# Kernel tuning notes

Hardware: AMD Instinct MI355X
Metric: run time of the kernel (lower is better)

## Reference

```python
import jax, jax.numpy as jnp
import numpy as np

LARGE_CONSTANT = 1e9


def setup_inputs() -> dict:
    key = jax.random.key(0)
    ks = jax.random.split(key, 8)
    B, S, D, U = 8, 2048, 1024, 1024
    scale = 1.0 / np.sqrt(D)
    inputs_1 = jax.random.normal(ks[0], (B, S, D), dtype=jnp.float32)
    inputs_2 = jax.random.normal(ks[1], (B, S, D), dtype=jnp.float32)
    Wq = jax.random.normal(ks[2], (D, U), dtype=jnp.float32) * scale
    Wk = jax.random.normal(ks[3], (D, U), dtype=jnp.float32) * scale
    Wv = jax.random.normal(ks[4], (D, U), dtype=jnp.float32) * scale
    bq = jnp.zeros((U,), dtype=jnp.float32)
    bk = jnp.zeros((U,), dtype=jnp.float32)
    bv = jnp.zeros((U,), dtype=jnp.float32)
    # metric initialized as identity in the original; add small noise to exercise it
    metric = jnp.eye(U, dtype=jnp.float32) + 0.01 * jax.random.normal(ks[5], (U, U), dtype=jnp.float32)
    return {"inputs_1": inputs_1, "inputs_2": inputs_2, "Wq": Wq, "bq": bq,
            "Wk": Wk, "bk": bk, "Wv": Wv, "bv": bv, "metric": metric}


def reference(inputs_1, inputs_2, Wq, bq, Wk, bk, Wv, bv, metric):
    U = Wq.shape[1]
    scaling = jnp.sqrt(jnp.asarray(U, dtype=inputs_1.dtype))
    queries = inputs_1 @ Wq + bq            # [b, i, u]
    keys = inputs_2 @ Wk + bk               # [b, j, u]
    values = inputs_2 @ Wv + bv             # [b, j, u]
    queries = jnp.einsum('biu,uv->biv', queries, metric)  # learned-metric transform
    scores = jnp.einsum('biu,bju->bij', queries, keys) / scaling
    # causal mask: band_part(ones, -1, 0) is lower-triangular
    S = scores.shape[-1]
    causal = jnp.tril(jnp.ones((S, S), dtype=scores.dtype))
    scores = scores - LARGE_CONSTANT * (1.0 - causal)
    alpha = jax.nn.softmax(scores, axis=-1)
    return jnp.einsum('bij,bju->biu', alpha, values)
```

## Files before the change

kernel.cpp:

```cpp
#include <hip/hip_runtime.h>


#define Bq 8
#define Sq 2048
#define Dq 1024
#define Uq 1024

typedef __bf16 bf16;
typedef __bf16 bf16x8 __attribute__((ext_vector_type(8)));
typedef float f32x4 __attribute__((ext_vector_type(4)));
typedef unsigned short u16;
typedef unsigned int u32;

__device__ __forceinline__ u16 f2bf(float f) {
  u32 u = __builtin_bit_cast(u32, f);
  u32 r = u + 0x7fffu + ((u >> 16) & 1u);
  return (u16)(r >> 16);
}
__device__ __forceinline__ float bf2f(u32 h) {
  return __builtin_bit_cast(float, h << 16);
}

__device__ __forceinline__ void gl_lds16(const void* g, void* l) {
  __builtin_amdgcn_global_load_lds(
      (const __attribute__((address_space(1))) u32*)g,
      (__attribute__((address_space(3))) u32*)l, 16, 0, 0);
}


__global__ __launch_bounds__(256) void cvt_x(const float* __restrict__ x1,
                                             const float* __restrict__ x2,
                                             u16* __restrict__ o1,
                                             u16* __restrict__ o2, int n4) {
  int idx = blockIdx.x * 256 + threadIdx.x;
  if (idx >= n4) return;
  const float* in = blockIdx.y ? x2 : x1;
  u16* out = blockIdx.y ? o2 : o1;
  float4 v = ((const float4*)in)[idx];
  ushort4 o;
  o.x = f2bf(v.x); o.y = f2bf(v.y); o.z = f2bf(v.z); o.w = f2bf(v.w);
  ((ushort4*)out)[idx] = o;
}

__global__ __launch_bounds__(256) void cvt_bf16(const float* __restrict__ in,
                                                u16* __restrict__ out, int n4) {
  int idx = blockIdx.x * 256 + threadIdx.x;
  if (idx >= n4) return;
  float4 v = ((const float4*)in)[idx];
  ushort4 o;
  o.x = f2bf(v.x); o.y = f2bf(v.y); o.z = f2bf(v.z); o.w = f2bf(v.w);
  ((ushort4*)out)[idx] = o;
}

__global__ __launch_bounds__(256) void transpose_cvt3(
    const float* __restrict__ s0, u16* __restrict__ d0,
    const float* __restrict__ s1, u16* __restrict__ d1,
    const float* __restrict__ s2, u16* __restrict__ d2) {
  __shared__ float tile[32][33];
  const float* in = (blockIdx.z == 0) ? s0 : (blockIdx.z == 1) ? s1 : s2;
  u16* out = (blockIdx.z == 0) ? d0 : (blockIdx.z == 1) ? d1 : d2;
  const int N = 1024;
  int tx = threadIdx.x & 31, ty = threadIdx.x >> 5;
  int x0 = blockIdx.x * 32, y0 = blockIdx.y * 32;
#pragma unroll
  for (int r = 0; r < 32; r += 8)
    tile[ty + r][tx] = in[(size_t)(y0 + ty + r) * N + x0 + tx];
  __syncthreads();
#pragma unroll
  for (int r = 0; r < 32; r += 8)
    out[(size_t)(x0 + ty + r) * N + y0 + tx] = f2bf(tile[tx][ty + r]);
}

__global__ __launch_bounds__(256) void bqm_kernel(const float* __restrict__ bq,
                                                  const float* __restrict__ metric,
                                                  float* __restrict__ bqm) {
  int v = blockIdx.x * 256 + threadIdx.x;
  float s = 0.f;
  for (int u = 0; u < Uq; ++u) s += bq[u] * metric[(size_t)u * Uq + v];
  bqm[v] = s;
}

__global__ __launch_bounds__(256) void fill_zero(float4* __restrict__ p, int n4) {
  int i = blockIdx.x * 256 + threadIdx.x;
  if (i < n4) p[i] = float4{0.f, 0.f, 0.f, 0.f};
}

#define BM 128
#define BN 128
#define BK 32

template <int OUT_BF16, int BIAS>
__global__ __launch_bounds__(256) void gemm_tn(
    const bf16* __restrict__ A, const bf16* __restrict__ B, void* __restrict__ Cv,
    const float* __restrict__ bias, int lda, int ldb, int ldc,
    long long sA, long long sB, long long sC, int K,
    int causal_skip, int causal_klimit) {
  __shared__ __align__(16) bf16 lA[3][BM * BK];
  __shared__ __align__(16) bf16 lB[3][BN * BK];
  int bx = causal_klimit ? (gridDim.x - 1 - blockIdx.x) : blockIdx.x;
  int m0 = bx * BM, n0 = blockIdx.y * BN;
  if (causal_skip && n0 > m0 + BM - 1) return;
  long long b = blockIdx.z;
  A += b * sA;
  B += b * sB;
  int t = threadIdx.x;
  int w = t >> 6, l = t & 63;
  int wr = (w >> 1) * 64, wc = (w & 1) * 64;
  int Kend = causal_klimit ? min(K, m0 + BM) : K;
  int nk = Kend / BK;

  f32x4 acc[4][4] = {};
  int rowA = t >> 2, kc = (t & 3) * 8;
  int lm = l & 15, q = l >> 4;

  const bf16* gA = A + (long long)(m0 + rowA) * lda + kc;
  const bf16* gB = B + (long long)(n0 + rowA) * ldb + kc;
  long long a64 = (long long)64 * lda, b64 = (long long)64 * ldb;

  auto stage = [&](int kt, int buf) {
    int k0 = kt * BK;
    char* dA = (char*)lA[buf] + w * 1024;
    char* dB = (char*)lB[buf] + w * 1024;
    gl_lds16(gA + k0, dA);
    gl_lds16(gA + k0 + a64, dA + 4096);
    gl_lds16(gB + k0, dB);
    gl_lds16(gB + k0 + b64, dB + 4096);
  };

  stage(0, 0);
  stage(1, 1);
  int cur = 0;
  for (int kt = 0; kt < nk; ++kt) {
    if (kt + 2 < nk) {
      int pb = cur + 2;
      if (pb >= 3) pb -= 3;
      stage(kt + 2, pb);
      asm volatile("s_waitcnt vmcnt(8)\n\ts_barrier" ::: "memory");
    } else if (kt + 1 < nk) {
      asm volatile("s_waitcnt vmcnt(4)\n\ts_barrier" ::: "memory");
    } else {
      asm volatile("s_waitcnt vmcnt(0)\n\ts_barrier" ::: "memory");
    }
    bf16x8 af[4], bfr[4];
#pragma unroll
    for (int i = 0; i < 4; ++i)
      af[i] = *(const bf16x8*)&lA[cur][(wr + i * 16 + lm) * BK + q * 8];
#pragma unroll
    for (int i = 0; i < 4; ++i)
      bfr[i] = *(const bf16x8*)&lB[cur][(wc + i * 16 + lm) * BK + q * 8];
#pragma unroll
    for (int i = 0; i < 4; ++i)
#pragma unroll
      for (int j = 0; j < 4; ++j)
        acc[i][j] = __builtin_amdgcn_mfma_f32_16x16x32_bf16(af[i], bfr[j], acc[i][j], 0, 0, 0);
    asm volatile("s_barrier" ::: "memory");
    cur = (cur == 2) ? 0 : cur + 1;
  }

  char* Cb = (char*)Cv + (OUT_BF16 ? b * sC * 2 : b * sC * 4);
#pragma unroll
  for (int i = 0; i < 4; ++i) {
#pragma unroll
    for (int j = 0; j < 4; ++j) {
      int col = n0 + wc + j * 16 + lm;
      float bc = (BIAS == 1) ? bias[col] : 0.f;
#pragma unroll
      for (int r = 0; r < 4; ++r) {
        int row = m0 + wr + i * 16 + q * 4 + r;
        float v = acc[i][j][r] + bc;
        if (BIAS == 2) v += bias[row];
        size_t idx = (size_t)row * ldc + col;
        if (OUT_BF16)
          ((u16*)Cb)[idx] = f2bf(v);
        else
          ((float*)Cb)[idx] = v;
      }
    }
  }
}


#define GBODY(P, CLO, CB, NLO, NB)                                             \
  {                                                                            \
    const int rp_ = (P) & 3, rn_ = ((P) + 1) & 3;                              \
    if ((P) + 3 < NP) stage((P) + 3);                                          \
    const bf16* pa_ = pAl + rp_ * 8192;                                        \
    _Pragma("unroll") for (int i = 0; i < 4; ++i)                              \
        aHi[i] = *(const bf16x8*)(pa_ + (i + 4) * 512);                        \
    __builtin_amdgcn_s_setprio(1);                                             \
    _Pragma("unroll") for (int i = 0; i < 4; ++i)                              \
        _Pragma("unroll") for (int j = 0; j < 4; ++j)                          \
            acc[i][j] = __builtin_amdgcn_mfma_f32_16x16x32_bf16(               \
                CLO[i], CB[j], acc[i][j], 0, 0, 0);                            \
    __builtin_amdgcn_s_setprio(0);                                             \
    if ((P) + 1 < NP) {                                                        \
      const bf16* pa2_ = pAl + rn_ * 8192;                                     \
      const bf16* pb2_ = pBl + rn_ * 8192;                                     \
      _Pragma("unroll") for (int i = 0; i < 4; ++i)                            \
          NLO[i] = *(const bf16x8*)(pa2_ + i * 512);                           \
      _Pragma("unroll") for (int j = 0; j < 4; ++j)                            \
          NB[j] = *(const bf16x8*)(pb2_ + j * 512);                            \
    }                                                                          \
    __builtin_amdgcn_s_setprio(1);                                             \
    _Pragma("unroll") for (int i = 0; i < 4; ++i)                              \
        _Pragma("unroll") for (int j = 0; j < 4; ++j)                          \
            acc[i + 4][j] = __builtin_amdgcn_mfma_f32_16x16x32_bf16(           \
                aHi[i], CB[j], acc[i + 4][j], 0, 0, 0);                        \
    __builtin_amdgcn_s_setprio(0);                                             \
    if ((P) + 3 < NP)                                                          \
      asm volatile("s_waitcnt vmcnt(4) lgkmcnt(0)\n\ts_barrier" ::: "memory"); \
    else if ((P) + 2 < NP)                                                     \
      asm volatile("s_waitcnt vmcnt(0) lgkmcnt(0)\n\ts_barrier" ::: "memory"); \
  }

template <int OUT_BF16, int BIAS>
__global__ __launch_bounds__(512, 2) void gemm_tn256(
    const bf16* __restrict__ A, const bf16* __restrict__ B, void* __restrict__ Cv,
    const float* __restrict__ bias, int lda, int ldb, int ldc,
    long long sA, long long sB, long long sC, int K,
    int causal_skip, int causal_klimit) {
  __shared__ __align__(16) bf16 lA[4][256 * 32];
  __shared__ __align__(16) bf16 lB[4][256 * 32];
  int bx = causal_klimit ? (gridDim.x - 1 - blockIdx.x) : blockIdx.x;
  int m0 = bx * 256, n0 = blockIdx.y * 256;
  if (causal_skip && n0 > m0 + 255) return;
  long long b = blockIdx.z;
  A += b * sA;
  B += b * sB;
  int t = threadIdx.x;
  int w = t >> 6, l = t & 63;
  int wr = w >> 2, wc = w & 3;
  int lm = l & 15, q = l >> 4;
  int cq = q ^ ((lm >> 1) & 3);

  int Kend = causal_klimit ? min(K, m0 + 256) : K;
  int NP = Kend >> 5;

  int r0 = t >> 2;
  int c0 = t & 3;
  int q0 = c0 ^ ((r0 >> 1) & 3);
  const bf16* gA0 = A + (long long)(m0 + r0) * lda + q0 * 8;
  const bf16* gA1 = gA0 + (long long)128 * lda;
  const bf16* gB0 = B + (long long)(n0 + r0) * ldb + q0 * 8;
  const bf16* gB1 = gB0 + (long long)128 * ldb;
  char* dA = (char*)&lA[0][0] + w * 1024;
  char* dB = (char*)&lB[0][0] + w * 1024;

  auto stage = [&](int ph) {
    int reg_ = ph & 3;
    int k0 = ph << 5;
    char* da = dA + reg_ * 16384;
    char* db = dB + reg_ * 16384;
    gl_lds16(gA0 + k0, da);
    gl_lds16(gA1 + k0, da + 8192);
    gl_lds16(gB0 + k0, db);
    gl_lds16(gB1 + k0, db + 8192);
  };

  const bf16* pAl = &lA[0][0] + (wr * 128 + lm) * 32 + cq * 8;
  const bf16* pBl = &lB[0][0] + (wc * 64 + lm) * 32 + cq * 8;

  f32x4 acc[8][4] = {};
  bf16x8 aLoA[4], bFrA[4], aLoB[4], bFrB[4], aHi[4];

  stage(0); stage(1); stage(2);
  asm volatile("s_waitcnt vmcnt(8)\n\ts_barrier" ::: "memory");
#pragma unroll
  for (int i = 0; i < 4; ++i) aLoA[i] = *(const bf16x8*)(pAl + i * 512);
#pragma unroll
  for (int j = 0; j < 4; ++j) bFrA[j] = *(const bf16x8*)(pBl + j * 512);
  asm volatile("s_waitcnt vmcnt(4) lgkmcnt(0)\n\ts_barrier" ::: "memory");

  for (int p = 0; p < NP; p += 2) {
    GBODY(p, aLoA, bFrA, aLoB, bFrB)
    GBODY(p + 1, aLoB, bFrB, aLoA, bFrA)
  }

  char* Cb = (char*)Cv + (OUT_BF16 ? b * sC * 2 : b * sC * 4);
#pragma unroll
  for (int i = 0; i < 8; ++i) {
#pragma unroll
    for (int j = 0; j < 4; ++j) {
      int col = n0 + wc * 64 + j * 16 + lm;
      float bc = (BIAS == 1) ? bias[col] : 0.f;
#pragma unroll
      for (int r = 0; r < 4; ++r) {
        int row = m0 + wr * 128 + i * 16 + q * 4 + r;
        float v = acc[i][j][r] + bc;
        if (BIAS == 2) v += bias[row];
        size_t idxc = (size_t)row * ldc + col;
        if (OUT_BF16)
          ((u16*)Cb)[idxc] = f2bf(v);
        else
          ((float*)Cb)[idxc] = v;
      }
    }
  }
}

__global__ __launch_bounds__(256) void softmax_causal(u16* __restrict__ sc) {
  __shared__ __align__(16) float sm[Sq];
  __shared__ float red[8];
  int gr = blockIdx.x;
  int i = gr & (Sq - 1);
  u16* rowp = sc + (size_t)gr * Sq;
  int t = threadIdx.x;
  int nv = i + 1;
  int wlim = (i & ~255) + 256;
  int j0 = t * 8;
  if (j0 < nv) {
    uint4 pk = ((const uint4*)rowp)[t];
    float4 lo, hi;
    lo.x = bf2f(pk.x & 0xffffu); lo.y = bf2f(pk.x >> 16);
    lo.z = bf2f(pk.y & 0xffffu); lo.w = bf2f(pk.y >> 16);
    hi.x = bf2f(pk.z & 0xffffu); hi.y = bf2f(pk.z >> 16);
    hi.z = bf2f(pk.w & 0xffffu); hi.w = bf2f(pk.w >> 16);
    ((float4*)sm)[2 * t] = lo;
    ((float4*)sm)[2 * t + 1] = hi;
  }
  __syncthreads();
  const float scl = 0.03125f;
  float m = -1e30f;
  for (int j = t; j < nv; j += 256) m = fmaxf(m, sm[j]);
#pragma unroll
  for (int o = 32; o; o >>= 1) m = fmaxf(m, __shfl_xor(m, o));
  if ((t & 63) == 0) red[t >> 6] = m;
  __syncthreads();
  m = fmaxf(fmaxf(red[0], red[1]), fmaxf(red[2], red[3])) * scl;
  float sum = 0.f;
  for (int j = t; j < nv; j += 256) sum += __expf(sm[j] * scl - m);
#pragma unroll
  for (int o = 32; o; o >>= 1) sum += __shfl_xor(sum, o);
  if ((t & 63) == 0) red[4 + (t >> 6)] = sum;
  __syncthreads();
  float rinv = 1.0f / (red[4] + red[5] + red[6] + red[7]);
  if (j0 < wlim) {
    u16 ov[8];
#pragma unroll
    for (int k = 0; k < 8; ++k)
      ov[k] = (j0 + k < nv) ? f2bf(__expf(sm[j0 + k] * scl - m) * rinv) : (u16)0;
    uint4 po;
    po.x = (u32)ov[0] | ((u32)ov[1] << 16);
    po.y = (u32)ov[2] | ((u32)ov[3] << 16);
    po.z = (u32)ov[4] | ((u32)ov[5] << 16);
    po.w = (u32)ov[6] | ((u32)ov[7] << 16);
    ((uint4*)rowp)[t] = po;
  }
}


extern "C" void kernel_launch(void* const* d_in, const int* in_sizes, int n_in,
                              void* d_out, int out_size, void* d_ws, size_t ws_size,
                              hipStream_t stream) {
  const float* X1 = (const float*)d_in[0];
  const float* X2 = (const float*)d_in[1];
  const float* Wq = (const float*)d_in[2];
  const float* bq = (const float*)d_in[3];
  const float* Wk = (const float*)d_in[4];
  const float* bk = (const float*)d_in[5];
  const float* Wv = (const float*)d_in[6];
  const float* bv = (const float*)d_in[7];
  const float* metric = (const float*)d_in[8];
  float* out = (float*)d_out;

  const size_t XB = (size_t)Bq * Sq * Dq * 2;
  const size_t WB = (size_t)Dq * Uq * 2;
  const size_t NEED = 3 * XB + 5 * WB + 4096;

  if (ws_size < NEED) {
    fill_zero<<<(out_size / 4 + 255) / 256, 256, 0, stream>>>((float4*)d_out, out_size / 4);
    return;
  }

  char* ws = (char*)d_ws;
  bf16* X1b = (bf16*)(ws);
  bf16* X2b = (bf16*)(ws + XB);
  bf16* Vt = (bf16*)(ws + 2 * XB);
  bf16* WqB = (bf16*)(ws + 3 * XB);
  bf16* metT = (bf16*)(ws + 3 * XB + WB);
  bf16* WkT = (bf16*)(ws + 3 * XB + 2 * WB);
  bf16* WvT = (bf16*)(ws + 3 * XB + 3 * WB);
  bf16* WqmT = (bf16*)(ws + 3 * XB + 4 * WB);
  float* bqm = (float*)(ws + 3 * XB + 5 * WB);
  u16* Sc = (u16*)ws;
  bf16* Qb = (bf16*)d_out;
  bf16* Kb = (bf16*)d_out + (size_t)Bq * Sq * Uq;

  int nx4 = Bq * Sq * Dq / 4;
  cvt_x<<<dim3((nx4 + 255) / 256, 2), 256, 0, stream>>>(X1, X2, (u16*)X1b, (u16*)X2b, nx4);
  cvt_bf16<<<(Dq * Uq / 4 + 255) / 256, 256, 0, stream>>>(Wq, (u16*)WqB, Dq * Uq / 4);
  transpose_cvt3<<<dim3(32, 32, 3), 256, 0, stream>>>(
      metric, (u16*)metT, Wk, (u16*)WkT, Wv, (u16*)WvT);
  bqm_kernel<<<Uq / 256, 256, 0, stream>>>(bq, metric, bqm);

  gemm_tn<1, 0><<<dim3(Uq / BM, Dq / BN, 1), 256, 0, stream>>>(
      metT, WqB, WqmT, nullptr, Uq, Uq, Dq, 0, 0, 0, Uq, 0, 0);

  const int MQ = Bq * Sq;
  gemm_tn256<1, 1><<<dim3(MQ / 256, Uq / 256, 1), 512, 0, stream>>>(
      X1b, WqmT, Qb, bqm, Dq, Dq, Uq, 0, 0, 0, Dq, 0, 0);
  gemm_tn256<1, 1><<<dim3(MQ / 256, Uq / 256, 1), 512, 0, stream>>>(
      X2b, WkT, Kb, bk, Dq, Dq, Uq, 0, 0, 0, Dq, 0, 0);
  gemm_tn256<1, 2><<<dim3(Uq / 256, Sq / 256, Bq), 512, 0, stream>>>(
      WvT, X2b, Vt, bv, Dq, Dq, Sq, 0, (long long)Sq * Dq, (long long)Uq * Sq, Dq, 0, 0);

  gemm_tn256<1, 0><<<dim3(Sq / 256, Sq / 256, Bq), 512, 0, stream>>>(
      Qb, Kb, Sc, nullptr, Uq, Uq, Sq, (long long)Sq * Uq, (long long)Sq * Uq,
      (long long)Sq * Sq, Uq, 1, 0);

  softmax_causal<<<Bq * Sq, 256, 0, stream>>>(Sc);

  gemm_tn256<0, 0><<<dim3(Sq / 256, Uq / 256, Bq), 512, 0, stream>>>(
      (const bf16*)Sc, Vt, out, nullptr, Sq, Sq, Uq, (long long)Sq * Sq,
      (long long)Uq * Sq, (long long)Sq * Uq, Sq, 0, 1);

  (void)in_sizes; (void)n_in; (void)ws_size;
}
```

Baseline: 524.5 us.

## Split global-to-LDS staging across half-phases and split-K the weight-fold GEMM

The 256-tile GEMM main loop now issues half of each prefetch stage before and half after the first MFMA group, and places barriers between the two halves of every phase with finer vmcnt waits. The loop is unrolled four phases deep with compile-time LDS region indices. The intent is to spread memory traffic and shorten barrier stalls. Separately, the small metric×Wq GEMM is split along K into four atomic-add slices into an fp32 buffer, then converted to bf16, to expose more parallelism. This adds a zero-fill kernel and a conversion kernel, plus atomic traffic.

```diff
diff --git a/kernel.cpp b/kernel.cpp
--- a/kernel.cpp
+++ b/kernel.cpp
@@ -157,7 +157,7 @@
     cur = (cur == 2) ? 0 : cur + 1;
   }
 
-  char* Cb = (char*)Cv + (OUT_BF16 ? b * sC * 2 : b * sC * 4);
+  char* Cb = (char*)Cv + (OUT_BF16 == 1 ? b * sC * 2 : b * sC * 4);
 #pragma unroll
   for (int i = 0; i < 4; ++i) {
 #pragma unroll
@@ -170,8 +170,10 @@
         float v = acc[i][j][r] + bc;
         if (BIAS == 2) v += bias[row];
         size_t idx = (size_t)row * ldc + col;
-        if (OUT_BF16)
+        if (OUT_BF16 == 1)
           ((u16*)Cb)[idx] = f2bf(v);
+        else if (OUT_BF16 == 2)
+          unsafeAtomicAdd(&((float*)Cb)[idx], v);
         else
           ((float*)Cb)[idx] = v;
       }
@@ -180,37 +182,48 @@
 }
 
 
-#define GBODY(P, CLO, CB, NLO, NB)                                             \
+#define PH(P, RG, CAL, CBF, NAL, NBF)                                          \
   {                                                                            \
-    const int rp_ = (P) & 3, rn_ = ((P) + 1) & 3;                              \
-    if ((P) + 3 < NP) stage((P) + 3);                                          \
-    const bf16* pa_ = pAl + rp_ * 8192;                                        \
+                                                           \
+    if ((P) + 3 < NP) {                                                        \
+      gl_lds16(gA0 + (((P) + 3) << 5), dA + (((RG) + 3) & 3) * 16384);         \
+      gl_lds16(gB0 + (((P) + 3) << 5), dB + (((RG) + 3) & 3) * 16384);         \
+    }                                                                          \
     _Pragma("unroll") for (int i = 0; i < 4; ++i)                              \
-        aHi[i] = *(const bf16x8*)(pa_ + (i + 4) * 512);                        \
+        aHi[i] = *(const bf16x8*)(pAl + (RG) * 8192 + (i + 4) * 512);          \
+    if ((P) + 3 < NP)                                                          \
+      asm volatile("s_waitcnt vmcnt(6)" ::: "memory");                         \
+    else if ((P) + 2 < NP)                                                     \
+      asm volatile("s_waitcnt vmcnt(4)" ::: "memory");                         \
+    else                                                                       \
+      asm volatile("s_waitcnt vmcnt(0)" ::: "memory");                         \
+    asm volatile("s_barrier" ::: "memory");                                    \
+    asm volatile("s_waitcnt lgkmcnt(0)" ::: "memory");                         \
     __builtin_amdgcn_s_setprio(1);                                             \
     _Pragma("unroll") for (int i = 0; i < 4; ++i)                              \
         _Pragma("unroll") for (int j = 0; j < 4; ++j)                          \
             acc[i][j] = __builtin_amdgcn_mfma_f32_16x16x32_bf16(               \
-                CLO[i], CB[j], acc[i][j], 0, 0, 0);                            \
+                CAL[i], CBF[j], acc[i][j], 0, 0, 0);                           \
     __builtin_amdgcn_s_setprio(0);                                             \
+                                                           \
+    if ((P) + 3 < NP) {                                                        \
+      gl_lds16(gA1 + (((P) + 3) << 5), dA + (((RG) + 3) & 3) * 16384 + 8192);  \
+      gl_lds16(gB1 + (((P) + 3) << 5), dB + (((RG) + 3) & 3) * 16384 + 8192);  \
+    }                                                                          \
     if ((P) + 1 < NP) {                                                        \
-      const bf16* pa2_ = pAl + rn_ * 8192;                                     \
-      const bf16* pb2_ = pBl + rn_ * 8192;                                     \
       _Pragma("unroll") for (int i = 0; i < 4; ++i)                            \
-          NLO[i] = *(const bf16x8*)(pa2_ + i * 512);                           \
+          NAL[i] = *(const bf16x8*)(pAl + (((RG) + 1) & 3) * 8192 + i * 512);  \
       _Pragma("unroll") for (int j = 0; j < 4; ++j)                            \
-          NB[j] = *(const bf16x8*)(pb2_ + j * 512);                            \
+          NBF[j] = *(const bf16x8*)(pBl + (((RG) + 1) & 3) * 8192 + j * 512);  \
     }                                                                          \
+    asm volatile("s_barrier" ::: "memory");                                    \
+    asm volatile("s_waitcnt lgkmcnt(0)" ::: "memory");                         \
     __builtin_amdgcn_s_setprio(1);                                             \
     _Pragma("unroll") for (int i = 0; i < 4; ++i)                              \
         _Pragma("unroll") for (int j = 0; j < 4; ++j)                          \
             acc[i + 4][j] = __builtin_amdgcn_mfma_f32_16x16x32_bf16(           \
-                aHi[i], CB[j], acc[i + 4][j], 0, 0, 0);                        \
+                aHi[i], CBF[j], acc[i + 4][j], 0, 0, 0);                       \
     __builtin_amdgcn_s_setprio(0);                                             \
-    if ((P) + 3 < NP)                                                          \
-      asm volatile("s_waitcnt vmcnt(4) lgkmcnt(0)\n\ts_barrier" ::: "memory"); \
-    else if ((P) + 2 < NP)                                                     \
-      asm volatile("s_waitcnt vmcnt(0) lgkmcnt(0)\n\ts_barrier" ::: "memory"); \
   }
 
 template <int OUT_BF16, int BIAS>
@@ -246,34 +259,37 @@
   char* dA = (char*)&lA[0][0] + w * 1024;
   char* dB = (char*)&lB[0][0] + w * 1024;
 
-  auto stage = [&](int ph) {
-    int reg_ = ph & 3;
-    int k0 = ph << 5;
-    char* da = dA + reg_ * 16384;
-    char* db = dB + reg_ * 16384;
-    gl_lds16(gA0 + k0, da);
-    gl_lds16(gA1 + k0, da + 8192);
-    gl_lds16(gB0 + k0, db);
-    gl_lds16(gB1 + k0, db + 8192);
-  };
-
   const bf16* pAl = &lA[0][0] + (wr * 128 + lm) * 32 + cq * 8;
   const bf16* pBl = &lB[0][0] + (wc * 64 + lm) * 32 + cq * 8;
 
   f32x4 acc[8][4] = {};
   bf16x8 aLoA[4], bFrA[4], aLoB[4], bFrB[4], aHi[4];
 
-  stage(0); stage(1); stage(2);
+  {
+    gl_lds16(gA0, dA);
+    gl_lds16(gA1, dA + 8192);
+    gl_lds16(gB0, dB);
+    gl_lds16(gB1, dB + 8192);
+    gl_lds16(gA0 + 32, dA + 16384);
+    gl_lds16(gA1 + 32, dA + 16384 + 8192);
+    gl_lds16(gB0 + 32, dB + 16384);
+    gl_lds16(gB1 + 32, dB + 16384 + 8192);
+    gl_lds16(gA0 + 64, dA + 32768);
+    gl_lds16(gA1 + 64, dA + 32768 + 8192);
+    gl_lds16(gB0 + 64, dB + 32768);
+    gl_lds16(gB1 + 64, dB + 32768 + 8192);
+  }
   asm volatile("s_waitcnt vmcnt(8)\n\ts_barrier" ::: "memory");
 #pragma unroll
   for (int i = 0; i < 4; ++i) aLoA[i] = *(const bf16x8*)(pAl + i * 512);
 #pragma unroll
   for (int j = 0; j < 4; ++j) bFrA[j] = *(const bf16x8*)(pBl + j * 512);
-  asm volatile("s_waitcnt vmcnt(4) lgkmcnt(0)\n\ts_barrier" ::: "memory");
-
-  for (int p = 0; p < NP; p += 2) {
-    GBODY(p, aLoA, bFrA, aLoB, bFrB)
-    GBODY(p + 1, aLoB, bFrB, aLoA, bFrA)
+
+  for (int p = 0; p < NP; p += 4) {
+    PH(p + 0, 0, aLoA, bFrA, aLoB, bFrB)
+    PH(p + 1, 1, aLoB, bFrB, aLoA, bFrA)
+    PH(p + 2, 2, aLoA, bFrA, aLoB, bFrB)
+    PH(p + 3, 3, aLoB, bFrB, aLoA, bFrA)
   }
 
   char* Cb = (char*)Cv + (OUT_BF16 ? b * sC * 2 : b * sC * 4);
@@ -383,6 +399,7 @@
   bf16* WqmT = (bf16*)(ws + 3 * XB + 4 * WB);
   float* bqm = (float*)(ws + 3 * XB + 5 * WB);
   u16* Sc = (u16*)ws;
+  float* WqmT_f32 = (float*)Vt;
   bf16* Qb = (bf16*)d_out;
   bf16* Kb = (bf16*)d_out + (size_t)Bq * Sq * Uq;
 
@@ -393,8 +410,10 @@
       metric, (u16*)metT, Wk, (u16*)WkT, Wv, (u16*)WvT);
   bqm_kernel<<<Uq / 256, 256, 0, stream>>>(bq, metric, bqm);
 
-  gemm_tn<1, 0><<<dim3(Uq / BM, Dq / BN, 1), 256, 0, stream>>>(
-      metT, WqB, WqmT, nullptr, Uq, Uq, Dq, 0, 0, 0, Uq, 0, 0);
+  fill_zero<<<Dq * Uq / 4 / 256, 256, 0, stream>>>((float4*)WqmT_f32, Dq * Uq / 4);
+  gemm_tn<2, 0><<<dim3(Uq / BM, Dq / BN, 4), 256, 0, stream>>>(
+      metT, WqB, WqmT_f32, nullptr, Uq, Uq, Dq, 256, 256, 0, 256, 0, 0);
+  cvt_bf16<<<(Dq * Uq / 4 + 255) / 256, 256, 0, stream>>>(WqmT_f32, (u16*)WqmT, Dq * Uq / 4);
 
   const int MQ = Bq * Sq;
   gemm_tn256<1, 1><<<dim3(MQ / 256, Uq / 256, 1), 512, 0, stream>>>(
```

After: 1.036 ms. 97.6% more time.
